# Kernel optimization log

Hardware: AMD Instinct MI355X
Metric: run time of the kernel (lower is better)

Reference implementation:

```python
import jax, jax.numpy as jnp
import numpy as np

B, N, L, F = 8, 256, 48, 96

def setup_inputs() -> dict:
    key = jax.random.key(0)
    k1, k2 = jax.random.split(key)
    x = jax.random.normal(k1, (B, N, N, L), dtype=jnp.float32)
    w = jax.random.normal(k2, (15, L, F), dtype=jnp.float32) * 0.05  # 'random_normal' init
    return {"x": x, "w": w}

def reference(x, w):
    # x: [B, N, N, L], w: [15, L, F]
    Bn, Nn, _, Ln = x.shape
    totsum = jnp.einsum('bijl->bl', x)          # [B, L]
    trace  = jnp.einsum('biil->bl', x)          # [B, L]
    diag   = jnp.einsum('biil->bil', x)         # [B, N, L]
    rowsum = jnp.einsum('bijl->bil', x)         # sum over j -> [B, N, L] (index i)
    colsum = jnp.einsum('bijl->bjl', x)         # sum over i -> [B, N, L] (index j)

    # Diagonal-placed terms (res0..res4): delta_ij * (node part + scalar part)
    diag_node = (jnp.einsum('bil,lf->bif', diag,   w[0])
               + jnp.einsum('bil,lf->bif', rowsum, w[1])
               + jnp.einsum('bil,lf->bif', colsum, w[2]))          # [B, N, F]
    diag_scal = trace @ w[3] + totsum @ w[4]                        # [B, F]
    eye = jnp.eye(Nn, dtype=x.dtype)
    out = (eye[None, :, :, None] * diag_node[:, :, None, :]
         + eye[None, :, :, None] * diag_scal[:, None, None, :])    # [B, N, N, F]

    # Broadcast over i (res5..res7: vector indexed by j)
    bj = (jnp.einsum('bjl,lf->bjf', diag,   w[5])
        + jnp.einsum('bjl,lf->bjf', rowsum, w[6])
        + jnp.einsum('bjl,lf->bjf', colsum, w[7]))                 # [B, N, F]
    out = out + bj[:, None, :, :]

    # Broadcast over j (res8..res10: vector indexed by i)
    bi = (jnp.einsum('bil,lf->bif', diag,   w[8])
        + jnp.einsum('bil,lf->bif', rowsum, w[9])
        + jnp.einsum('bil,lf->bif', colsum, w[10]))                # [B, N, F]
    out = out + bi[:, :, None, :]

    # Dense terms: transpose (res11) and identity (res12)
    out = out + jnp.einsum('bijl,lf->bjif', x, w[11])
    out = out + jnp.einsum('bijl,lf->bijf', x, w[12])

    # Global scalar broadcasts (res13, res14)
    scal = trace @ w[13] + totsum @ w[14]                           # [B, F]
    out = out + scal[:, None, None, :]
    return out
```

## Files before the change

kernel.cpp:

```cpp
#include <hip/hip_runtime.h>

#define Bx 8
#define Nx 256
#define Lx 48
#define Fx 96
#define KP 104

typedef __attribute__((ext_vector_type(8))) short bf16x8;
typedef __attribute__((ext_vector_type(4))) float f32x4;

__device__ __forceinline__ unsigned short f2bf(float f) {
    unsigned int u = __float_as_uint(f);
    u += 0x7fffu + ((u >> 16) & 1u);
    return (unsigned short)(u >> 16);
}
__device__ __forceinline__ unsigned int cvt_pk_bf16(float a, float b) {
    unsigned int r;
    asm("v_cvt_pk_bf16_f32 %0, %1, %2" : "=v"(r) : "v"(a), "v"(b));
    return r;
}

__global__ __launch_bounds__(192) void kA_fused(const float* __restrict__ x,
                                                const float* __restrict__ w,
                                                float* __restrict__ rowsum,
                                                float* __restrict__ colsum,
                                                float* __restrict__ diagv,
                                                float* __restrict__ trace,
                                                float* __restrict__ totsum,
                                                unsigned short* __restrict__ wt) {
    const int blk = blockIdx.x;
    const int t = threadIdx.x;
    if (blk < Bx * Nx) {
        __shared__ float red[192];
        const int l = t % Lx;
        const int g = t / Lx;
        const int b = blk >> 8;
        const size_t base = (size_t)blk * Nx * Lx;
        float acc = 0.f;
        for (int j = g; j < Nx; j += 4)
            acc += x[base + (size_t)j * Lx + l];
        red[t] = acc;
        __syncthreads();
        if (g == 0) {
            const float rs = red[l] + red[48 + l] + red[96 + l] + red[144 + l];
            rowsum[(size_t)blk * Lx + l] = rs;
            atomicAdd(totsum + b * Lx + l, rs);
        }
        if (t < Lx) {
            const float dv = x[base + (size_t)(blk & 255) * Lx + t];
            diagv[(size_t)blk * Lx + t] = dv;
            atomicAdd(trace + b * Lx + t, dv);
        }
    } else if (blk < Bx * Nx + 1024) {
        const int c  = blk - Bx * Nx;
        const int is = c & 7;
        const int jc = (c >> 3) & 15;
        const int b  = c >> 7;
        const size_t cb = (size_t)b * Nx * Nx * Lx + (size_t)jc * 16 * Lx;
        float a0 = 0.f, a1 = 0.f, a2 = 0.f, a3 = 0.f;
        for (int ii = 0; ii < 32; ++ii) {
            const float* p = x + cb + (size_t)(is * 32 + ii) * Nx * Lx;
            a0 += p[t];
            a1 += p[t + 192];
            a2 += p[t + 384];
            a3 += p[t + 576];
        }
        float* cp = colsum + ((size_t)b * Nx + jc * 16) * Lx;
        atomicAdd(cp + t,       a0);
        atomicAdd(cp + t + 192, a1);
        atomicAdd(cp + t + 384, a2);
        atomicAdd(cp + t + 576, a3);
    } else {
        const int idx = (blk - (Bx * Nx + 1024)) * 192 + t;
        const int f = idx / KP, kk = idx % KP;
        float v = 0.f;
        if (kk < 48)      v = w[12 * Lx * Fx + kk * Fx + f];
        else if (kk < 96) v = w[11 * Lx * Fx + (kk - 48) * Fx + f];
        wt[idx] = f2bf(v);
    }
}

__global__ __launch_bounds__(192) void k2_vectors(const float* __restrict__ w,
                                                  const float* __restrict__ rowsum,
                                                  const float* __restrict__ colsum,
                                                  const float* __restrict__ diagv,
                                                  const float* __restrict__ trace,
                                                  const float* __restrict__ totsum,
                                                  float* __restrict__ add_i,
                                                  float* __restrict__ add_j,
                                                  float* __restrict__ add_d) {
    const int blk = blockIdx.x;
    const int t = threadIdx.x;
    const int f  = t % Fx;
    const int nh = t / Fx;
    const int b  = blk >> 6;
    const int nb = b * Nx + (blk & 63) * 4 + nh * 2;
    const float* trP = trace  + b * Lx;
    const float* tsP = totsum + b * Lx;

    float ai[2] = {0.f, 0.f}, aj[2] = {0.f, 0.f}, ad[2] = {0.f, 0.f};
    float sd = 0.f, si = 0.f;
    for (int l = 0; l < Lx; ++l) {
        const float* wl = w + (size_t)l * Fx + f;
        const float w0  = wl[0];
        const float w1  = wl[1  * Lx * Fx];
        const float w2  = wl[2  * Lx * Fx];
        const float w3  = wl[3  * Lx * Fx];
        const float w4  = wl[4  * Lx * Fx];
        const float w5  = wl[5  * Lx * Fx];
        const float w6  = wl[6  * Lx * Fx];
        const float w7  = wl[7  * Lx * Fx];
        const float w8  = wl[8  * Lx * Fx];
        const float w9  = wl[9  * Lx * Fx];
        const float w10 = wl[10 * Lx * Fx];
        const float w13 = wl[13 * Lx * Fx];
        const float w14 = wl[14 * Lx * Fx];
        const float tr = trP[l], ts = tsP[l];
        sd = fmaf(tr, w3,  sd); sd = fmaf(ts, w4,  sd);
        si = fmaf(tr, w13, si); si = fmaf(ts, w14, si);
        #pragma unroll
        for (int nn = 0; nn < 2; ++nn) {
            const size_t ix = (size_t)(nb + nn) * Lx + l;
            const float d = diagv[ix], r = rowsum[ix], c = colsum[ix];
            ad[nn] = fmaf(d, w0, ad[nn]); ad[nn] = fmaf(r, w1, ad[nn]); ad[nn] = fmaf(c, w2,  ad[nn]);
            aj[nn] = fmaf(d, w5, aj[nn]); aj[nn] = fmaf(r, w6, aj[nn]); aj[nn] = fmaf(c, w7,  aj[nn]);
            ai[nn] = fmaf(d, w8, ai[nn]); ai[nn] = fmaf(r, w9, ai[nn]); ai[nn] = fmaf(c, w10, ai[nn]);
        }
    }
    #pragma unroll
    for (int nn = 0; nn < 2; ++nn) {
        const size_t idx = (size_t)(nb + nn) * Fx + f;
        add_d[idx] = ad[nn] + sd;
        add_j[idx] = aj[nn];
        add_i[idx] = ai[nn] + si;
    }
}

__global__ __launch_bounds__(256) void k3_mfma(const float* __restrict__ x,
                                               const unsigned short* __restrict__ wt,
                                               const float* __restrict__ add_i,
                                               const float* __restrict__ add_j,
                                               const float* __restrict__ add_d,
                                               float* __restrict__ out) {
    __shared__ unsigned short Al[64 * KP];
    __shared__ unsigned short Bl[96 * KP];
    const int rawx = blockIdx.x;
    const int idx  = (rawx & 7) * 80 + (rawx >> 3);
    const int b    = blockIdx.y;
    const int p    = idx >> 6;
    const int io   = idx & 63;
    int It, Jt;
    if (p < 4)      { It = 0; Jt = p; }
    else if (p < 7) { It = 1; Jt = p - 3; }
    else if (p < 9) { It = 2; Jt = p - 5; }
    else            { It = 3; Jt = 3; }
    const int i  = It * 64 + io;
    const int J  = Jt * 64;
    const int bi = b * Nx + i;
    const int t  = threadIdx.x;

    {
        const uint4* src = (const uint4*)wt;
        uint4* dst = (uint4*)Bl;
        #pragma unroll
        for (int it = 0; it < 5; ++it) {
            const int k = t + it * 256;
            if (k < (96 * KP * 2) / 16) dst[k] = src[k];
        }
    }
    {
        const int r = t >> 2, q = t & 3;
        const float* pij = x + ((size_t)bi * Nx + J + r) * Lx;
        const float* pji = x + ((size_t)(b * Nx + J + r) * Nx + i) * Lx;
        unsigned int* arow = (unsigned int*)Al + r * (KP / 2);
        #pragma unroll
        for (int e = 0; e < 3; ++e) {
            const float4 v = *(const float4*)(pij + q * 4 + e * 16);
            arow[q * 2 + e * 8 + 0] = cvt_pk_bf16(v.x, v.y);
            arow[q * 2 + e * 8 + 1] = cvt_pk_bf16(v.z, v.w);
        }
        #pragma unroll
        for (int e = 0; e < 3; ++e) {
            const float4 v = *(const float4*)(pji + q * 4 + e * 16);
            arow[24 + q * 2 + e * 8 + 0] = cvt_pk_bf16(v.x, v.y);
            arow[24 + q * 2 + e * 8 + 1] = cvt_pk_bf16(v.z, v.w);
        }
    }
    __syncthreads();

    const int wave = t >> 6, lane = t & 63;
    const int lm = lane & 15, quad = lane >> 4;
    const int m0 = wave * 16;
    const bool offd = (It != Jt);

    const float* aiP = add_i + (size_t)bi * Fx;
    const float* ajP = add_j + (size_t)bi * Fx;
    const float* adP = add_d + (size_t)bi * Fx;
    float* outP = out + (size_t)bi * Nx * Fx;

    bf16x8 afr0[3], afr1[3];
    #pragma unroll
    for (int ks = 0; ks < 3; ++ks) {
        const int off = ks * 32 + quad * 8;
        afr0[ks] = *(const bf16x8*)(Al + (m0 + lm) * KP + off);
    }
    if (offd) {
        #pragma unroll
        for (int ks = 0; ks < 3; ++ks) {
            const int off  = ks * 32 + quad * 8;
            const int offm = (off < 48) ? off + 48 : off - 48;
            afr1[ks] = *(const bf16x8*)(Al + (m0 + lm) * KP + offm);
        }
    }

    const int jbase = J + m0 + quad * 4;
    #pragma unroll
    for (int nt = 0; nt < 6; ++nt) {
        bf16x8 bfr[3];
        #pragma unroll
        for (int ks = 0; ks < 3; ++ks)
            bfr[ks] = *(const bf16x8*)(Bl + (nt * 16 + lm) * KP + ks * 32 + quad * 8);
        const int f = nt * 16 + lm;

        f32x4 c0 = {0.f, 0.f, 0.f, 0.f};
        #pragma unroll
        for (int ks = 0; ks < 3; ++ks)
            c0 = __builtin_amdgcn_mfma_f32_16x16x32_bf16(afr0[ks], bfr[ks], c0, 0, 0, 0);
        {
            const float ai = aiP[f];
            const float* ajRow = add_j + ((size_t)(b * Nx) + jbase) * Fx + f;
            #pragma unroll
            for (int reg = 0; reg < 4; ++reg) {
                float v = c0[reg] + ai + ajRow[(size_t)reg * Fx];
                if (!offd && (jbase + reg == i)) v += adP[f];
                __builtin_nontemporal_store(v, outP + (size_t)(jbase + reg) * Fx + f);
            }
        }
        if (offd) {
            f32x4 c1 = {0.f, 0.f, 0.f, 0.f};
            #pragma unroll
            for (int ks = 0; ks < 3; ++ks)
                c1 = __builtin_amdgcn_mfma_f32_16x16x32_bf16(afr1[ks], bfr[ks], c1, 0, 0, 0);
            const float aj = ajP[f];
            const float* aiRow = add_i + ((size_t)(b * Nx) + jbase) * Fx + f;
            float* op = out + ((size_t)(b * Nx + jbase) * Nx + i) * Fx + f;
            #pragma unroll
            for (int reg = 0; reg < 4; ++reg) {
                const float v = c1[reg] + aj + aiRow[(size_t)reg * Fx];
                __builtin_nontemporal_store(v, op + (size_t)reg * Nx * Fx);
            }
        }
    }
}

extern "C" void kernel_launch(void* const* d_in, const int* in_sizes, int n_in,
                              void* d_out, int out_size, void* d_ws, size_t ws_size,
                              hipStream_t stream) {
    const float* x = (const float*)d_in[0];
    const float* w = (const float*)d_in[1];
    float* out = (float*)d_out;

    float* ws      = (float*)d_ws;
    float* colsum  = ws;
    float* trace   = colsum + (size_t)Bx * Nx * Lx;
    float* totsum  = trace  + (size_t)Bx * Lx;
    float* rowsum  = totsum + (size_t)Bx * Lx;
    float* diagv   = rowsum + (size_t)Bx * Nx * Lx;
    float* add_i   = diagv  + (size_t)Bx * Nx * Lx;
    float* add_j   = add_i  + (size_t)Bx * Nx * Fx;
    float* add_d   = add_j  + (size_t)Bx * Nx * Fx;
    unsigned short* wtbf = (unsigned short*)(add_d + (size_t)Bx * Nx * Fx);

    hipMemsetAsync(ws, 0, ((size_t)Bx * Nx * Lx + 2 * Bx * Lx) * sizeof(float), stream);
    kA_fused<<<Bx * Nx + 1024 + 52, 192, 0, stream>>>(x, w, rowsum, colsum, diagv,
                                                      trace, totsum, wtbf);
    k2_vectors<<<512, 192, 0, stream>>>(w, rowsum, colsum, diagv, trace, totsum,
                                        add_i, add_j, add_d);
    dim3 g3(640, Bx);
    k3_mfma<<<g3, 256, 0, stream>>>(x, wtbf, add_i, add_j, add_d, out);
}
```

Before: 378.7 us.

## Fuse row and column sums into one pass over x, vectorize MFMA stores

Replaces the separate rowsum and colsum reductions, which each read x, with a single pass where each block reads four i-rows as float4. It produces rowsums and per-block partial column sums, and the column-sum atomics are dropped. k2 then reduces the 64 partials per column from a workspace in place of reading colsum. The MFMA operands are swapped so each lane holds four consecutive f outputs, which allows float4 loads of the add vectors and 16-byte nontemporal stores. The cost is a large partial-sum workspace (about 25 MB) written and re-read, and fewer blocks in the reduction kernel.

```diff
diff --git a/kernel.cpp b/kernel.cpp
--- a/kernel.cpp
+++ b/kernel.cpp
@@ -23,55 +23,64 @@
 __global__ __launch_bounds__(192) void kA_fused(const float* __restrict__ x,
                                                 const float* __restrict__ w,
                                                 float* __restrict__ rowsum,
-                                                float* __restrict__ colsum,
+                                                float* __restrict__ part,
                                                 float* __restrict__ diagv,
                                                 float* __restrict__ trace,
                                                 float* __restrict__ totsum,
                                                 unsigned short* __restrict__ wt) {
     const int blk = blockIdx.x;
     const int t = threadIdx.x;
-    if (blk < Bx * Nx) {
-        __shared__ float red[192];
-        const int l = t % Lx;
-        const int g = t / Lx;
-        const int b = blk >> 8;
-        const size_t base = (size_t)blk * Nx * Lx;
-        float acc = 0.f;
-        for (int j = g; j < Nx; j += 4)
-            acc += x[base + (size_t)j * Lx + l];
-        red[t] = acc;
+    if (blk < 512) {
+        const int b  = blk >> 6;
+        const int ic = blk & 63;
+        const int i0 = ic * 4;
+        const int jg = t / 12;
+        const int l4 = (t % 12) * 4;
+        const size_t xb = ((size_t)(b * Nx + i0)) * Nx * Lx;
+        float* __restrict__ pp = part + ((size_t)(ic * 8 + b)) * (Nx * Lx);
+
+        float4 r0 = {0.f,0.f,0.f,0.f}, r1 = r0, r2 = r0, r3 = r0;
+        #pragma unroll
+        for (int it = 0; it < 16; ++it) {
+            const int j = jg + 16 * it;
+            const size_t off = (size_t)j * Lx + l4;
+            const float4 v0 = *(const float4*)(x + xb + off);
+            const float4 v1 = *(const float4*)(x + xb + (size_t)Nx * Lx + off);
+            const float4 v2 = *(const float4*)(x + xb + 2 * (size_t)Nx * Lx + off);
+            const float4 v3 = *(const float4*)(x + xb + 3 * (size_t)Nx * Lx + off);
+            r0.x += v0.x; r0.y += v0.y; r0.z += v0.z; r0.w += v0.w;
+            r1.x += v1.x; r1.y += v1.y; r1.z += v1.z; r1.w += v1.w;
+            r2.x += v2.x; r2.y += v2.y; r2.z += v2.z; r2.w += v2.w;
+            r3.x += v3.x; r3.y += v3.y; r3.z += v3.z; r3.w += v3.w;
+            float4 cs;
+            cs.x = (v0.x + v1.x) + (v2.x + v3.x);
+            cs.y = (v0.y + v1.y) + (v2.y + v3.y);
+            cs.z = (v0.z + v1.z) + (v2.z + v3.z);
+            cs.w = (v0.w + v1.w) + (v2.w + v3.w);
+            *(float4*)(pp + off) = cs;
+        }
+        __shared__ float4 red[768];
+        red[        t] = r0;
+        red[192  + t] = r1;
+        red[384  + t] = r2;
+        red[576  + t] = r3;
         __syncthreads();
-        if (g == 0) {
-            const float rs = red[l] + red[48 + l] + red[96 + l] + red[144 + l];
-            rowsum[(size_t)blk * Lx + l] = rs;
-            atomicAdd(totsum + b * Lx + l, rs);
-        }
-        if (t < Lx) {
-            const float dv = x[base + (size_t)(blk & 255) * Lx + t];
-            diagv[(size_t)blk * Lx + t] = dv;
-            atomicAdd(trace + b * Lx + t, dv);
-        }
-    } else if (blk < Bx * Nx + 1024) {
-        const int c  = blk - Bx * Nx;
-        const int is = c & 7;
-        const int jc = (c >> 3) & 15;
-        const int b  = c >> 7;
-        const size_t cb = (size_t)b * Nx * Nx * Lx + (size_t)jc * 16 * Lx;
-        float a0 = 0.f, a1 = 0.f, a2 = 0.f, a3 = 0.f;
-        for (int ii = 0; ii < 32; ++ii) {
-            const float* p = x + cb + (size_t)(is * 32 + ii) * Nx * Lx;
-            a0 += p[t];
-            a1 += p[t + 192];
-            a2 += p[t + 384];
-            a3 += p[t + 576];
-        }
-        float* cp = colsum + ((size_t)b * Nx + jc * 16) * Lx;
-        atomicAdd(cp + t,       a0);
-        atomicAdd(cp + t + 192, a1);
-        atomicAdd(cp + t + 384, a2);
-        atomicAdd(cp + t + 576, a3);
+        {
+            const int r = t / 48, l = t % 48;
+            const float* rr = (const float*)(red + r * 192);
+            float s = 0.f;
+            #pragma unroll
+            for (int g = 0; g < 16; ++g)
+                s += rr[(g * 12 + (l >> 2)) * 4 + (l & 3)];
+            const size_t ri = ((size_t)(b * Nx + i0 + r)) * Lx + l;
+            rowsum[ri] = s;
+            atomicAdd(totsum + b * Lx + l, s);
+            const float dv = x[(((size_t)(b * Nx + i0 + r)) * Nx + (i0 + r)) * Lx + l];
+            diagv[ri] = dv;
+            atomicAdd(trace + b * Lx + l, dv);
+        }
     } else {
-        const int idx = (blk - (Bx * Nx + 1024)) * 192 + t;
+        const int idx = (blk - 512) * 192 + t;
         const int f = idx / KP, kk = idx % KP;
         float v = 0.f;
         if (kk < 48)      v = w[12 * Lx * Fx + kk * Fx + f];
@@ -82,7 +91,7 @@
 
 __global__ __launch_bounds__(192) void k2_vectors(const float* __restrict__ w,
                                                   const float* __restrict__ rowsum,
-                                                  const float* __restrict__ colsum,
+                                                  const float* __restrict__ part,
                                                   const float* __restrict__ diagv,
                                                   const float* __restrict__ trace,
                                                   const float* __restrict__ totsum,
@@ -91,10 +100,22 @@
                                                   float* __restrict__ add_d) {
     const int blk = blockIdx.x;
     const int t = threadIdx.x;
+    const int b  = blk >> 6;
+    const int n0 = (blk & 63) * 4;
+    __shared__ float csh[192];
+    {
+        const size_t e0 = (size_t)n0 * Lx + t;
+        float s = 0.f;
+        #pragma unroll 8
+        for (int ic = 0; ic < 64; ++ic)
+            s += part[((size_t)(ic * 8 + b)) * (Nx * Lx) + e0];
+        csh[t] = s;
+    }
+    __syncthreads();
+
     const int f  = t % Fx;
     const int nh = t / Fx;
-    const int b  = blk >> 6;
-    const int nb = b * Nx + (blk & 63) * 4 + nh * 2;
+    const int nb = b * Nx + n0 + nh * 2;
     const float* trP = trace  + b * Lx;
     const float* tsP = totsum + b * Lx;
 
@@ -121,7 +142,8 @@
         #pragma unroll
         for (int nn = 0; nn < 2; ++nn) {
             const size_t ix = (size_t)(nb + nn) * Lx + l;
-            const float d = diagv[ix], r = rowsum[ix], c = colsum[ix];
+            const float d = diagv[ix], r = rowsum[ix];
+            const float c = csh[(nh * 2 + nn) * Lx + l];
             ad[nn] = fmaf(d, w0, ad[nn]); ad[nn] = fmaf(r, w1, ad[nn]); ad[nn] = fmaf(c, w2,  ad[nn]);
             aj[nn] = fmaf(d, w5, aj[nn]); aj[nn] = fmaf(r, w6, aj[nn]); aj[nn] = fmaf(c, w7,  aj[nn]);
             ai[nn] = fmaf(d, w8, ai[nn]); ai[nn] = fmaf(r, w9, ai[nn]); ai[nn] = fmaf(c, w10, ai[nn]);
@@ -190,65 +212,70 @@
 
     const int wave = t >> 6, lane = t & 63;
     const int lm = lane & 15, quad = lane >> 4;
-    const int m0 = wave * 16;
+    const int n0 = wave * 16;
     const bool offd = (It != Jt);
+    const int j = J + n0 + lm;
 
     const float* aiP = add_i + (size_t)bi * Fx;
     const float* ajP = add_j + (size_t)bi * Fx;
     const float* adP = add_d + (size_t)bi * Fx;
     float* outP = out + (size_t)bi * Nx * Fx;
+    const bool isdiag = (!offd) && (j == i);
 
     bf16x8 afr0[3], afr1[3];
     #pragma unroll
     for (int ks = 0; ks < 3; ++ks) {
         const int off = ks * 32 + quad * 8;
-        afr0[ks] = *(const bf16x8*)(Al + (m0 + lm) * KP + off);
+        afr0[ks] = *(const bf16x8*)(Al + (n0 + lm) * KP + off);
     }
     if (offd) {
         #pragma unroll
         for (int ks = 0; ks < 3; ++ks) {
             const int off  = ks * 32 + quad * 8;
             const int offm = (off < 48) ? off + 48 : off - 48;
-            afr1[ks] = *(const bf16x8*)(Al + (m0 + lm) * KP + offm);
-        }
-    }
-
-    const int jbase = J + m0 + quad * 4;
+            afr1[ks] = *(const bf16x8*)(Al + (n0 + lm) * KP + offm);
+        }
+    }
+
     #pragma unroll
     for (int nt = 0; nt < 6; ++nt) {
         bf16x8 bfr[3];
         #pragma unroll
         for (int ks = 0; ks < 3; ++ks)
             bfr[ks] = *(const bf16x8*)(Bl + (nt * 16 + lm) * KP + ks * 32 + quad * 8);
-        const int f = nt * 16 + lm;
+        const int f0 = nt * 16 + quad * 4;
 
         f32x4 c0 = {0.f, 0.f, 0.f, 0.f};
         #pragma unroll
         for (int ks = 0; ks < 3; ++ks)
-            c0 = __builtin_amdgcn_mfma_f32_16x16x32_bf16(afr0[ks], bfr[ks], c0, 0, 0, 0);
+            c0 = __builtin_amdgcn_mfma_f32_16x16x32_bf16(bfr[ks], afr0[ks], c0, 0, 0, 0);
         {
-            const float ai = aiP[f];
-            const float* ajRow = add_j + ((size_t)(b * Nx) + jbase) * Fx + f;
-            #pragma unroll
-            for (int reg = 0; reg < 4; ++reg) {
-                float v = c0[reg] + ai + ajRow[(size_t)reg * Fx];
-                if (!offd && (jbase + reg == i)) v += adP[f];
-                __builtin_nontemporal_store(v, outP + (size_t)(jbase + reg) * Fx + f);
+            const float4 ai4 = *(const float4*)(aiP + f0);
+            const float4 aj4 = *(const float4*)(add_j + ((size_t)(b * Nx) + j) * Fx + f0);
+            f32x4 o;
+            o[0] = c0[0] + ai4.x + aj4.x;
+            o[1] = c0[1] + ai4.y + aj4.y;
+            o[2] = c0[2] + ai4.z + aj4.z;
+            o[3] = c0[3] + ai4.w + aj4.w;
+            if (isdiag) {
+                const float4 ad4 = *(const float4*)(adP + f0);
+                o[0] += ad4.x; o[1] += ad4.y; o[2] += ad4.z; o[3] += ad4.w;
             }
+            __builtin_nontemporal_store(o, (f32x4*)(outP + (size_t)j * Fx + f0));
         }
         if (offd) {
             f32x4 c1 = {0.f, 0.f, 0.f, 0.f};
             #pragma unroll
             for (int ks = 0; ks < 3; ++ks)
-                c1 = __builtin_amdgcn_mfma_f32_16x16x32_bf16(afr1[ks], bfr[ks], c1, 0, 0, 0);
-            const float aj = ajP[f];
-            const float* aiRow = add_i + ((size_t)(b * Nx) + jbase) * Fx + f;
-            float* op = out + ((size_t)(b * Nx + jbase) * Nx + i) * Fx + f;
-            #pragma unroll
-            for (int reg = 0; reg < 4; ++reg) {
-                const float v = c1[reg] + aj + aiRow[(size_t)reg * Fx];
-                __builtin_nontemporal_store(v, op + (size_t)reg * Nx * Fx);
-            }
+                c1 = __builtin_amdgcn_mfma_f32_16x16x32_bf16(bfr[ks], afr1[ks], c1, 0, 0, 0);
+            const float4 aj4 = *(const float4*)(ajP + f0);
+            const float4 ai4 = *(const float4*)(add_i + ((size_t)(b * Nx) + j) * Fx + f0);
+            f32x4 o;
+            o[0] = c1[0] + aj4.x + ai4.x;
+            o[1] = c1[1] + aj4.y + ai4.y;
+            o[2] = c1[2] + aj4.z + ai4.z;
+            o[3] = c1[3] + aj4.w + ai4.w;
+            __builtin_nontemporal_store(o, (f32x4*)(out + ((size_t)(b * Nx + j) * Nx + i) * Fx + f0));
         }
     }
 }
@@ -261,20 +288,20 @@
     float* out = (float*)d_out;
 
     float* ws      = (float*)d_ws;
-    float* colsum  = ws;
-    float* trace   = colsum + (size_t)Bx * Nx * Lx;
+    float* trace   = ws;
     float* totsum  = trace  + (size_t)Bx * Lx;
     float* rowsum  = totsum + (size_t)Bx * Lx;
     float* diagv   = rowsum + (size_t)Bx * Nx * Lx;
-    float* add_i   = diagv  + (size_t)Bx * Nx * Lx;
+    float* part    = diagv  + (size_t)Bx * Nx * Lx;
+    float* add_i   = part   + (size_t)512 * Nx * Lx;
     float* add_j   = add_i  + (size_t)Bx * Nx * Fx;
     float* add_d   = add_j  + (size_t)Bx * Nx * Fx;
     unsigned short* wtbf = (unsigned short*)(add_d + (size_t)Bx * Nx * Fx);
 
-    hipMemsetAsync(ws, 0, ((size_t)Bx * Nx * Lx + 2 * Bx * Lx) * sizeof(float), stream);
-    kA_fused<<<Bx * Nx + 1024 + 52, 192, 0, stream>>>(x, w, rowsum, colsum, diagv,
-                                                      trace, totsum, wtbf);
-    k2_vectors<<<512, 192, 0, stream>>>(w, rowsum, colsum, diagv, trace, totsum,
+    (void)hipMemsetAsync(ws, 0, (size_t)2 * Bx * Lx * sizeof(float), stream);
+    kA_fused<<<512 + 52, 192, 0, stream>>>(x, w, rowsum, part, diagv,
+                                           trace, totsum, wtbf);
+    k2_vectors<<<512, 192, 0, stream>>>(w, rowsum, part, diagv, trace, totsum,
                                         add_i, add_j, add_d);
     dim3 g3(640, Bx);
     k3_mfma<<<g3, 256, 0, stream>>>(x, wtbf, add_i, add_j, add_d, out);
```

New measurement: 367.8 us. 2.9% less time.
